# Kernel optimization log

Hardware: AMD Instinct MI355X
Metric: run time of the kernel (lower is better)

The kernel has to match this reference:

```python
import jax, jax.numpy as jnp
import numpy as np

COMMITMENT_COST = 0.25


def setup_inputs() -> dict:
    key = jax.random.key(0)
    k1, k2 = jax.random.split(key)
    inputs = jax.random.normal(k1, (16, 4096, 256), dtype=jnp.float32)
    codewords = jax.random.normal(k2, (1024, 256), dtype=jnp.float32)
    return {"inputs": inputs, "codewords": codewords}


def reference(inputs, codewords):
    # inputs: (*, D), codewords: (K, D)
    D = codewords.shape[-1]
    flat = inputs.reshape(-1, D)  # (N, D)
    x_sq = jnp.sum(flat * flat, axis=-1, keepdims=True)            # (N, 1)
    c_sq = jnp.sum(codewords * codewords, axis=-1)                 # (K,)
    distances = x_sq - 2.0 * (flat @ codewords.T) + c_sq           # (N, K)
    encoding_indices = jnp.argmin(distances, axis=1)               # (N,)
    quantized = codewords[encoding_indices].reshape(inputs.shape)  # (*, D)
    # Straight-through estimator
    quantized_st = inputs + jax.lax.stop_gradient(quantized - inputs)
    quantizing_loss = jnp.mean((quantized_st - jax.lax.stop_gradient(inputs)) ** 2)
    commitment_loss = jnp.mean((jax.lax.stop_gradient(quantized_st) - inputs) ** 2)
    loss = quantizing_loss + COMMITMENT_COST * commitment_loss
    return quantized_st, encoding_indices.reshape(inputs.shape[:-1]), loss
```

## Files before the change

### kernel.cpp

```cpp
#include <hip/hip_runtime.h>
#include <math.h>

typedef _Float16 v8h __attribute__((ext_vector_type(8)));
typedef float v4f __attribute__((ext_vector_type(4)));

constexpr int D      = 256;
constexpr int NTILE  = 64;
constexpr int KS     = 8;
constexpr int TILE_B = 8192;
constexpr int WIN_B  = 16384;
#define GUARD 2.0f

__global__ void vq_prep(const float* __restrict__ cw, unsigned short* __restrict__ img) {
    int gid = blockIdx.x * 256 + threadIdx.x;
    int t  = gid >> 9;
    int r  = gid & 511;
    int ks = r >> 6;
    int l  = r & 63;
    int cand = t * 16 + (l & 15);
    int k0   = ks * 32 + (l >> 4) * 8;
    const float* src = cw + (size_t)cand * D + k0;
    float4 t0 = *(const float4*)(src);
    float4 t1 = *(const float4*)(src + 4);
    v8h h;
    h[0] = (_Float16)t0.x; h[1] = (_Float16)t0.y;
    h[2] = (_Float16)t0.z; h[3] = (_Float16)t0.w;
    h[4] = (_Float16)t1.x; h[5] = (_Float16)t1.y;
    h[6] = (_Float16)t1.z; h[7] = (_Float16)t1.w;
    *(v8h*)((char*)img + (size_t)gid * 16) = h;
}

__global__ void vq_csq(const float* __restrict__ cw, float* __restrict__ csq) {
    int k = blockIdx.x * blockDim.x + threadIdx.x;
    const float4* p = reinterpret_cast<const float4*>(cw + (size_t)k * D);
    float s = 0.f;
    #pragma unroll 8
    for (int i = 0; i < D / 4; ++i) {
        float4 v = p[i];
        s += v.x * v.x; s += v.y * v.y; s += v.z * v.z; s += v.w * v.w;
    }
    csq[k] = s;
}

__launch_bounds__(256, 2)
__global__ void vq_main(const float* __restrict__ inp,
                        const float* __restrict__ cw,
                        const unsigned short* __restrict__ img,
                        const float* __restrict__ csq,
                        float* __restrict__ outq,
                        float* __restrict__ outi,
                        float* __restrict__ bsum) {
    __shared__ char  smem[2][WIN_B];
    __shared__ int4  s_pack[128];
    __shared__ float s_xsq[128];
    __shared__ int   s_win[128];
    __shared__ float s_l[4];

    const int tid  = threadIdx.x;
    const int lane = tid & 63;
    const int w    = tid >> 6;
    const int lr   = lane & 15;
    const int q    = lane >> 4;
    const int base = blockIdx.x * 128 + w * 32;

    #pragma unroll
    for (int i = 0; i < 4; ++i) {
        int off = i * 4096 + w * 1024;
        __builtin_amdgcn_global_load_lds(
            (const __attribute__((address_space(1))) unsigned int*)((const char*)img + off + lane * 16),
            (__attribute__((address_space(3))) unsigned int*)(&smem[0][off]),
            16, 0, 0);
    }

    v8h a2[2][8];
    #pragma unroll
    for (int m = 0; m < 2; ++m) {
        const float* rp = inp + (size_t)(base + m * 16 + lr) * D + q * 8;
        float sq = 0.f;
        #pragma unroll
        for (int ks = 0; ks < KS; ++ks) {
            float4 t0 = *(const float4*)(rp + ks * 32);
            float4 t1 = *(const float4*)(rp + ks * 32 + 4);
            sq = fmaf(t0.x, t0.x, sq); sq = fmaf(t0.y, t0.y, sq);
            sq = fmaf(t0.z, t0.z, sq); sq = fmaf(t0.w, t0.w, sq);
            sq = fmaf(t1.x, t1.x, sq); sq = fmaf(t1.y, t1.y, sq);
            sq = fmaf(t1.z, t1.z, sq); sq = fmaf(t1.w, t1.w, sq);
            v8h h;
            h[0] = (_Float16)(-2.f * t0.x); h[1] = (_Float16)(-2.f * t0.y);
            h[2] = (_Float16)(-2.f * t0.z); h[3] = (_Float16)(-2.f * t0.w);
            h[4] = (_Float16)(-2.f * t1.x); h[5] = (_Float16)(-2.f * t1.y);
            h[6] = (_Float16)(-2.f * t1.z); h[7] = (_Float16)(-2.f * t1.w);
            a2[m][ks] = h;
        }
        sq += __shfl_xor(sq, 16);
        sq += __shfl_xor(sq, 32);
        if (q == 0) s_xsq[w * 32 + m * 16 + lr] = sq;
    }

    const float BIGF = __uint_as_float(0x7F000000u);
    float v1[2][4], v2[2][4];
    #pragma unroll
    for (int m = 0; m < 2; ++m)
        #pragma unroll
        for (int r = 0; r < 4; ++r) { v1[m][r] = BIGF; v2[m][r] = BIGF; }

    asm volatile("s_waitcnt vmcnt(0)" ::: "memory");
    __builtin_amdgcn_s_barrier();
    __builtin_amdgcn_sched_barrier(0);

    int cur = 0;
    for (int win = 0; win < NTILE / 2; ++win) {
        if (win + 1 < NTILE / 2) {
            const char* srct = (const char*)img + (size_t)(win + 1) * WIN_B;
            #pragma unroll
            for (int i = 0; i < 4; ++i) {
                int off = i * 4096 + w * 1024;
                __builtin_amdgcn_global_load_lds(
                    (const __attribute__((address_space(1))) unsigned int*)(srct + off + lane * 16),
                    (__attribute__((address_space(3))) unsigned int*)(&smem[cur ^ 1][off]),
                    16, 0, 0);
            }
        }
        float cqA = csq[(2 * win) * 16 + lr] + 4096.f;
        float cqB = csq[(2 * win + 1) * 16 + lr] + 4096.f;

        const char* bb = smem[cur];
        v4f aA0 = {cqA, cqA, cqA, cqA}; v4f aA1 = aA0;
        v4f aB0 = {cqB, cqB, cqB, cqB}; v4f aB1 = aB0;
        #pragma unroll
        for (int ks = 0; ks < KS; ++ks) {
            v8h bA = *(const v8h*)(bb + ks * 1024 + lane * 16);
            v8h bB = *(const v8h*)(bb + TILE_B + ks * 1024 + lane * 16);
            aA0 = __builtin_amdgcn_mfma_f32_16x16x32_f16(a2[0][ks], bA, aA0, 0, 0, 0);
            aB0 = __builtin_amdgcn_mfma_f32_16x16x32_f16(a2[0][ks], bB, aB0, 0, 0, 0);
            aA1 = __builtin_amdgcn_mfma_f32_16x16x32_f16(a2[1][ks], bA, aA1, 0, 0, 0);
            aB1 = __builtin_amdgcn_mfma_f32_16x16x32_f16(a2[1][ks], bB, aB1, 0, 0, 0);
        }
        unsigned idxA = (unsigned)((2 * win) * 16) | (unsigned)lr;
        unsigned idxB = (unsigned)((2 * win + 1) * 16) | (unsigned)lr;
        #pragma unroll
        for (int r = 0; r < 4; ++r) {
            float f;
            f = __uint_as_float(((__float_as_uint(aA0[r]) + 0x200u) & 0xFFFFFC00u) | idxA);
            { float mx = fmaxf(v1[0][r], f); v2[0][r] = fminf(v2[0][r], mx); v1[0][r] = fminf(v1[0][r], f); }
            f = __uint_as_float(((__float_as_uint(aA1[r]) + 0x200u) & 0xFFFFFC00u) | idxA);
            { float mx = fmaxf(v1[1][r], f); v2[1][r] = fminf(v2[1][r], mx); v1[1][r] = fminf(v1[1][r], f); }
            f = __uint_as_float(((__float_as_uint(aB0[r]) + 0x200u) & 0xFFFFFC00u) | idxB);
            { float mx = fmaxf(v1[0][r], f); v2[0][r] = fminf(v2[0][r], mx); v1[0][r] = fminf(v1[0][r], f); }
            f = __uint_as_float(((__float_as_uint(aB1[r]) + 0x200u) & 0xFFFFFC00u) | idxB);
            { float mx = fmaxf(v1[1][r], f); v2[1][r] = fminf(v2[1][r], mx); v1[1][r] = fminf(v1[1][r], f); }
        }

        asm volatile("s_waitcnt vmcnt(0)" ::: "memory");
        __builtin_amdgcn_s_barrier();
        __builtin_amdgcn_sched_barrier(0);
        cur ^= 1;
    }

    #pragma unroll
    for (int m = 0; m < 2; ++m)
        #pragma unroll
        for (int r = 0; r < 4; ++r) {
            float L0 = v1[m][r], L1 = v2[m][r], L2 = BIGF, L3 = BIGF;
            #pragma unroll
            for (int off = 8; off; off >>= 1) {
                float P0 = __shfl_xor(L0, off, 16);
                float P1 = __shfl_xor(L1, off, 16);
                float P2 = __shfl_xor(L2, off, 16);
                float P3 = __shfl_xor(L3, off, 16);
                float M0 = fminf(L0, P3), M1 = fminf(L1, P2);
                float M2 = fminf(L2, P1), M3 = fminf(L3, P0);
                float a0 = fminf(M0, M2), c0 = fmaxf(M0, M2);
                float b0 = fminf(M1, M3), d0 = fmaxf(M1, M3);
                L0 = fminf(a0, b0); L1 = fmaxf(a0, b0);
                L2 = fminf(c0, d0); L3 = fmaxf(c0, d0);
            }
            if (lr == 0) {
                int rloc = m * 16 + q * 4 + r;
                s_pack[w * 32 + rloc] = make_int4(
                    (int)__float_as_uint(L0), (int)__float_as_uint(L1),
                    (int)__float_as_uint(L2), (int)__float_as_uint(L3));
            }
        }

    const int c = lane & 3;
    float lacc = 0.f;
    #pragma unroll
    for (int h = 0; h < 2; ++h) {
        int rloc = h * 16 + (lane >> 2);
        int grow = base + rloc;
        int4 pk = s_pack[w * 32 + rloc];
        float L0 = __uint_as_float((unsigned)pk.x);
        float L1 = __uint_as_float((unsigned)pk.y);
        float L2 = __uint_as_float((unsigned)pk.z);
        float L3 = __uint_as_float((unsigned)pk.w);
        float xq = s_xsq[w * 32 + rloc];

        int   bi;
        float bd;
        bool rescue = (L1 - L0) < GUARD;
        if (rescue) {
            float Lc = (c == 0) ? L0 : (c == 1) ? L1 : (c == 2) ? L2 : L3;
            int cd = (int)(__float_as_uint(Lc) & 1023u);
            const float4* xp = (const float4*)(inp + (size_t)grow * D);
            const float4* cp = (const float4*)(cw + (size_t)cd * D);
            float dot = 0.f, xsq = 0.f;
            #pragma unroll 8
            for (int i = 0; i < D / 4; ++i) {
                float4 xv = xp[i];
                float4 cv = cp[i];
                xsq = fmaf(xv.x, xv.x, xsq);
                xsq = fmaf(xv.y, xv.y, xsq);
                xsq = fmaf(xv.z, xv.z, xsq);
                xsq = fmaf(xv.w, xv.w, xsq);
                dot = fmaf(xv.x, cv.x, dot);
                dot = fmaf(xv.y, cv.y, dot);
                dot = fmaf(xv.z, cv.z, dot);
                dot = fmaf(xv.w, cv.w, dot);
            }
            float m2 = dot + dot;
            float t  = xsq - m2;
            float e  = t + csq[cd];
            bd = e; bi = cd;
            #pragma unroll
            for (int off = 1; off <= 2; off <<= 1) {
                float ev = __shfl_xor(bd, off, 4);
                int   iv = __shfl_xor(bi, off, 4);
                bool  tk = (ev < bd) || (ev == bd && iv < bi);
                bd = tk ? ev : bd;
                bi = tk ? iv : bi;
            }
        } else {
            bi = (int)(__float_as_uint(L0) & 1023u);
            bd = (L0 - 4096.f) + xq;
        }

        if (c == 0) { s_win[w * 32 + rloc] = bi; lacc += bd; }
    }

    #pragma unroll 4
    for (int rr = 0; rr < 32; ++rr) {
        int bw = s_win[w * 32 + rr];
        float4 cv = *(const float4*)(cw + (size_t)bw * D + lane * 4);
        *(float4*)(outq + (size_t)(base + rr) * D + lane * 4) = cv;
        if (lane == 0) outi[base + rr] = (float)bw;
    }

    #pragma unroll
    for (int off = 32; off; off >>= 1) lacc += __shfl_xor(lacc, off);
    if (lane == 0) s_l[w] = lacc;
    __syncthreads();
    if (tid == 0) bsum[blockIdx.x] = s_l[0] + s_l[1] + s_l[2] + s_l[3];
}

__global__ void vq_finalize(const float* __restrict__ bsum, float* __restrict__ out_loss,
                            int nb, float scale) {
    __shared__ float s[4];
    int tid = threadIdx.x;
    float v = 0.f;
    for (int i = tid; i < nb; i += 256) v += bsum[i];
    #pragma unroll
    for (int off = 32; off; off >>= 1) v += __shfl_down(v, off, 64);
    if ((tid & 63) == 0) s[tid >> 6] = v;
    __syncthreads();
    if (tid == 0) out_loss[0] = (s[0] + s[1] + s[2] + s[3]) * scale;
}

extern "C" void kernel_launch(void* const* d_in, const int* in_sizes, int n_in,
                              void* d_out, int out_size, void* d_ws, size_t ws_size,
                              hipStream_t stream) {
    const float* inp = (const float*)d_in[0];
    const float* cw  = (const float*)d_in[1];
    float* out = (float*)d_out;
    const int N = in_sizes[0] / D;
    const int K = in_sizes[1] / D;

    char* ws = (char*)d_ws;
    unsigned short* img = (unsigned short*)ws;
    float* csq  = (float*)(ws + (size_t)K * D * 2);
    float* bsum = csq + K;

    float* outq = out;
    float* outi = out + (size_t)N * D;
    float* outl = outi + N;

    vq_prep<<<dim3((K * 32) / 256), dim3(256), 0, stream>>>(cw, img);
    vq_csq<<<dim3(K / 256), dim3(256), 0, stream>>>(cw, csq);

    vq_main<<<dim3(N / 128), dim3(256), 0, stream>>>(inp, cw, img, csq,
                                                     outq, outi, bsum);
    vq_finalize<<<dim3(1), dim3(256), 0, stream>>>(bsum, outl, N / 128,
                                                   1.25f / ((float)N * (float)D));
}
```

Baseline: 96.58 us.

## Triple-buffer codeword tiles with one barrier per window and cache csq in LDS

Replaces the double-buffered codeword pipeline with a three-stage LDS ring. Each iteration waits for the older prefetch with a partial vmcnt, issues one barrier, then prefetches two windows ahead, so the end-of-iteration full wait is gone. It also preloads the codeword norms into LDS once, raises wave priority around the MFMA block, and lowers the GUARD constant. The extra 16KB LDS buffer plus 4KB for norms may reduce occupancy at two blocks per CU, and the GUARD change may affect the tie-breaking refinement.

```diff
diff --git a/kernel.cpp b/kernel.cpp
--- a/kernel.cpp
+++ b/kernel.cpp
@@ -5,11 +5,12 @@
 typedef float v4f __attribute__((ext_vector_type(4)));
 
 constexpr int D      = 256;
-constexpr int NTILE  = 64;
 constexpr int KS     = 8;
 constexpr int TILE_B = 8192;
+constexpr int TPW    = 2;
 constexpr int WIN_B  = 16384;
-#define GUARD 2.0f
+constexpr int NWIN   = 32;
+#define GUARD 1.0f
 
 __global__ void vq_prep(const float* __restrict__ cw, unsigned short* __restrict__ img) {
     int gid = blockIdx.x * 256 + threadIdx.x;
@@ -50,7 +51,8 @@
                         float* __restrict__ outq,
                         float* __restrict__ outi,
                         float* __restrict__ bsum) {
-    __shared__ char  smem[2][WIN_B];
+    __shared__ __align__(16) char smem[3][WIN_B];
+    __shared__ float s_cq[1024];
     __shared__ int4  s_pack[128];
     __shared__ float s_xsq[128];
     __shared__ int   s_win[128];
@@ -63,13 +65,28 @@
     const int q    = lane >> 4;
     const int base = blockIdx.x * 128 + w * 32;
 
-    #pragma unroll
-    for (int i = 0; i < 4; ++i) {
-        int off = i * 4096 + w * 1024;
-        __builtin_amdgcn_global_load_lds(
-            (const __attribute__((address_space(1))) unsigned int*)((const char*)img + off + lane * 16),
-            (__attribute__((address_space(3))) unsigned int*)(&smem[0][off]),
-            16, 0, 0);
+#define VQ_STAGE(WIN, BUF)                                                           \
+    {                                                                                \
+        const char* srct = (const char*)img + (size_t)(WIN) * WIN_B;                 \
+        _Pragma("unroll")                                                            \
+        for (int i = 0; i < 4; ++i) {                                                \
+            int off = i * 4096 + w * 1024;                                           \
+            __builtin_amdgcn_global_load_lds(                                        \
+                (const __attribute__((address_space(1))) unsigned int*)(srct + off + lane * 16), \
+                (__attribute__((address_space(3))) unsigned int*)(&smem[BUF][off]),  \
+                16, 0, 0);                                                           \
+        }                                                                            \
+    }
+
+    VQ_STAGE(0, 0)
+    VQ_STAGE(1, 1)
+
+    {
+        float4 cv4 = ((const float4*)csq)[tid];
+        s_cq[tid * 4 + 0] = cv4.x + 4096.f;
+        s_cq[tid * 4 + 1] = cv4.y + 4096.f;
+        s_cq[tid * 4 + 2] = cv4.z + 4096.f;
+        s_cq[tid * 4 + 3] = cv4.w + 4096.f;
     }
 
     v8h a2[2][8];
@@ -104,58 +121,60 @@
         #pragma unroll
         for (int r = 0; r < 4; ++r) { v1[m][r] = BIGF; v2[m][r] = BIGF; }
 
+    __syncthreads();
+
+#define VQ_COMPUTE(BUF, WIN)                                                         \
+    {                                                                                \
+        float cq0 = s_cq[(2 * (WIN)) * 16 + lr];                                     \
+        float cq1 = s_cq[(2 * (WIN) + 1) * 16 + lr];                                 \
+        v4f a00 = {cq0, cq0, cq0, cq0}; v4f a01 = a00;                               \
+        v4f a10 = {cq1, cq1, cq1, cq1}; v4f a11 = a10;                               \
+        const char* bb = smem[BUF];                                                  \
+        __builtin_amdgcn_s_setprio(1);                                               \
+        _Pragma("unroll")                                                            \
+        for (int ks = 0; ks < KS; ++ks) {                                            \
+            v8h b0 = *(const v8h*)(bb + ks * 1024 + lane * 16);                      \
+            v8h b1 = *(const v8h*)(bb + TILE_B + ks * 1024 + lane * 16);             \
+            a00 = __builtin_amdgcn_mfma_f32_16x16x32_f16(a2[0][ks], b0, a00, 0, 0, 0); \
+            a10 = __builtin_amdgcn_mfma_f32_16x16x32_f16(a2[0][ks], b1, a10, 0, 0, 0); \
+            a01 = __builtin_amdgcn_mfma_f32_16x16x32_f16(a2[1][ks], b0, a01, 0, 0, 0); \
+            a11 = __builtin_amdgcn_mfma_f32_16x16x32_f16(a2[1][ks], b1, a11, 0, 0, 0); \
+        }                                                                            \
+        __builtin_amdgcn_s_setprio(0);                                               \
+        unsigned idx0 = (unsigned)((2 * (WIN)) * 16) | (unsigned)lr;                 \
+        unsigned idx1 = (unsigned)((2 * (WIN) + 1) * 16) | (unsigned)lr;             \
+        _Pragma("unroll")                                                            \
+        for (int r = 0; r < 4; ++r) {                                                \
+            float f;                                                                 \
+            f = __uint_as_float(((__float_as_uint(a00[r]) + 0x200u) & 0xFFFFFC00u) | idx0); \
+            { float mx = fmaxf(v1[0][r], f); v2[0][r] = fminf(v2[0][r], mx); v1[0][r] = fminf(v1[0][r], f); } \
+            f = __uint_as_float(((__float_as_uint(a01[r]) + 0x200u) & 0xFFFFFC00u) | idx0); \
+            { float mx = fmaxf(v1[1][r], f); v2[1][r] = fminf(v2[1][r], mx); v1[1][r] = fminf(v1[1][r], f); } \
+            f = __uint_as_float(((__float_as_uint(a10[r]) + 0x200u) & 0xFFFFFC00u) | idx1); \
+            { float mx = fmaxf(v1[0][r], f); v2[0][r] = fminf(v2[0][r], mx); v1[0][r] = fminf(v1[0][r], f); } \
+            f = __uint_as_float(((__float_as_uint(a11[r]) + 0x200u) & 0xFFFFFC00u) | idx1); \
+            { float mx = fmaxf(v1[1][r], f); v2[1][r] = fminf(v2[1][r], mx); v1[1][r] = fminf(v1[1][r], f); } \
+        }                                                                            \
+    }
+
+    int cm = 0;
+    int st = 2;
+    for (int win = 0; win < NWIN - 1; ++win) {
+        asm volatile("s_waitcnt vmcnt(4)" ::: "memory");
+        __builtin_amdgcn_s_barrier();
+        __builtin_amdgcn_sched_barrier(0);
+        if (win + 2 < NWIN) VQ_STAGE(win + 2, st)
+        __builtin_amdgcn_sched_barrier(0);
+        VQ_COMPUTE(cm, win)
+        cm = (cm == 2) ? 0 : cm + 1;
+        st = (st == 2) ? 0 : st + 1;
+    }
     asm volatile("s_waitcnt vmcnt(0)" ::: "memory");
     __builtin_amdgcn_s_barrier();
     __builtin_amdgcn_sched_barrier(0);
-
-    int cur = 0;
-    for (int win = 0; win < NTILE / 2; ++win) {
-        if (win + 1 < NTILE / 2) {
-            const char* srct = (const char*)img + (size_t)(win + 1) * WIN_B;
-            #pragma unroll
-            for (int i = 0; i < 4; ++i) {
-                int off = i * 4096 + w * 1024;
-                __builtin_amdgcn_global_load_lds(
-                    (const __attribute__((address_space(1))) unsigned int*)(srct + off + lane * 16),
-                    (__attribute__((address_space(3))) unsigned int*)(&smem[cur ^ 1][off]),
-                    16, 0, 0);
-            }
-        }
-        float cqA = csq[(2 * win) * 16 + lr] + 4096.f;
-        float cqB = csq[(2 * win + 1) * 16 + lr] + 4096.f;
-
-        const char* bb = smem[cur];
-        v4f aA0 = {cqA, cqA, cqA, cqA}; v4f aA1 = aA0;
-        v4f aB0 = {cqB, cqB, cqB, cqB}; v4f aB1 = aB0;
-        #pragma unroll
-        for (int ks = 0; ks < KS; ++ks) {
-            v8h bA = *(const v8h*)(bb + ks * 1024 + lane * 16);
-            v8h bB = *(const v8h*)(bb + TILE_B + ks * 1024 + lane * 16);
-            aA0 = __builtin_amdgcn_mfma_f32_16x16x32_f16(a2[0][ks], bA, aA0, 0, 0, 0);
-            aB0 = __builtin_amdgcn_mfma_f32_16x16x32_f16(a2[0][ks], bB, aB0, 0, 0, 0);
-            aA1 = __builtin_amdgcn_mfma_f32_16x16x32_f16(a2[1][ks], bA, aA1, 0, 0, 0);
-            aB1 = __builtin_amdgcn_mfma_f32_16x16x32_f16(a2[1][ks], bB, aB1, 0, 0, 0);
-        }
-        unsigned idxA = (unsigned)((2 * win) * 16) | (unsigned)lr;
-        unsigned idxB = (unsigned)((2 * win + 1) * 16) | (unsigned)lr;
-        #pragma unroll
-        for (int r = 0; r < 4; ++r) {
-            float f;
-            f = __uint_as_float(((__float_as_uint(aA0[r]) + 0x200u) & 0xFFFFFC00u) | idxA);
-            { float mx = fmaxf(v1[0][r], f); v2[0][r] = fminf(v2[0][r], mx); v1[0][r] = fminf(v1[0][r], f); }
-            f = __uint_as_float(((__float_as_uint(aA1[r]) + 0x200u) & 0xFFFFFC00u) | idxA);
-            { float mx = fmaxf(v1[1][r], f); v2[1][r] = fminf(v2[1][r], mx); v1[1][r] = fminf(v1[1][r], f); }
-            f = __uint_as_float(((__float_as_uint(aB0[r]) + 0x200u) & 0xFFFFFC00u) | idxB);
-            { float mx = fmaxf(v1[0][r], f); v2[0][r] = fminf(v2[0][r], mx); v1[0][r] = fminf(v1[0][r], f); }
-            f = __uint_as_float(((__float_as_uint(aB1[r]) + 0x200u) & 0xFFFFFC00u) | idxB);
-            { float mx = fmaxf(v1[1][r], f); v2[1][r] = fminf(v2[1][r], mx); v1[1][r] = fminf(v1[1][r], f); }
-        }
-
-        asm volatile("s_waitcnt vmcnt(0)" ::: "memory");
-        __builtin_amdgcn_s_barrier();
-        __builtin_amdgcn_sched_barrier(0);
-        cur ^= 1;
-    }
+    VQ_COMPUTE(cm, NWIN - 1)
+#undef VQ_COMPUTE
+#undef VQ_STAGE
 
     #pragma unroll
     for (int m = 0; m < 2; ++m)
```

Result: faster. 91.10 us (-5.7%).
